# Kernel tuning notes

Hardware: AMD Instinct MI355X
Metric: run time of the kernel (lower is better)

## Reference

```python
import jax, jax.numpy as jnp
import numpy as np

B, CI, H, W = 128, 16, 32, 32
CO, K, S = 32, 3, 1
HO = (H - K) // S + 1  # 30
WO = (W - K) // S + 1  # 30
P = HO * WO  # 900 spatial locations
B_J0 = 0.1
DT = 0.5
BETA_ADAPT = 1.8  # is_adapt=True
BN_EPS = 1e-5


def setup_inputs() -> dict:
    key = jax.random.key(0)
    ks = jax.random.split(key, 16)
    inp = {
        'ff': jax.random.normal(ks[0], (B, CI, H, W), jnp.float32),
        'fb': jax.random.normal(ks[1], (B, CO, HO, WO), jnp.float32),
        'soma_t': jax.random.normal(ks[2], (B, CO, HO, WO), jnp.float32),
        'spk_t': (jax.random.uniform(ks[3], (B, CO, HO, WO)) > 0.7).astype(jnp.float32),
        'a_curr_t': jax.random.normal(ks[4], (B, CO, HO, WO), jnp.float32),
        'b_t': jax.random.uniform(ks[5], (B, CO, HO, WO), jnp.float32),
        # parameters
        'weight': jax.random.normal(ks[6], (1, CO, CI, HO, WO, K * K), jnp.float32) * 0.05,
        'conv_bias': jnp.zeros((1, CO, HO, WO), jnp.float32),
        'local_rec': jax.random.normal(ks[7], (P, CO, CO), jnp.float32) * (1.0 / np.sqrt(2.0 * CO)),
        'gamma': jnp.ones((CO,), jnp.float32),
        'beta': jnp.zeros((CO,), jnp.float32),
        'tau_m': 15.0 + 0.1 * jax.random.normal(ks[8], (CO, HO, WO), jnp.float32),
        'tau_adp': 20.0 + 0.1 * jax.random.normal(ks[9], (CO, HO, WO), jnp.float32),
        'tau_a': 15.0 + 0.1 * jax.random.normal(ks[10], (CO, HO, WO), jnp.float32),
    }
    return inp


def local_conv(x, weight, bias):
    # torch unfold(2,k).unfold(3,k) order: (kh, kw) fastest -> [B,Ci,Ho,Wo,k*k]
    patches = jnp.stack(
        [x[:, :, i:i + S * HO:S, j:j + S * WO:S] for i in range(K) for j in range(K)],
        axis=-1)
    out = jnp.einsum('bchwk,ochwk->bohw', patches, weight[0])
    return out + bias


def reference(ff, fb, soma_t, spk_t, a_curr_t, b_t, weight, conv_bias,
              local_rec, gamma, beta, tau_m, tau_adp, tau_a):
    # locally-connected conv + BatchNorm2d (training mode: batch stats)
    conv = local_conv(ff, weight, conv_bias)
    mean = conv.mean(axis=(0, 2, 3), keepdims=True)
    var = ((conv - mean) ** 2).mean(axis=(0, 2, 3), keepdims=True)  # biased var
    x = (conv - mean) * jax.lax.rsqrt(var + BN_EPS)
    conv_x = x * gamma[None, :, None, None] + beta[None, :, None, None]
    # recurrent per-location bmm: local_rec [P,Co,Co] @ spk [P,Co,B]
    spk_flat = spk_t.reshape(B, CO, P)
    rec = jnp.einsum('pij,bjp->bip', local_rec, spk_flat).reshape(B, CO, HO, WO)
    conv_x = conv_x + rec
    # adaptive LIF membrane update
    alpha = jnp.exp(-DT / tau_m)
    rho = jnp.exp(-DT / tau_adp)
    eta = jnp.exp(-DT / tau_a)
    b_new = rho * b_t + (1.0 - rho) * spk_t
    new_thre = B_J0 + BETA_ADAPT * b_new
    a_new = eta * a_curr_t + fb
    soma_new = alpha * soma_t + (jax.nn.sigmoid(a_new) - 0.5) + conv_x - new_thre * spk_t
    spike = (soma_new - new_thre > 0).astype(soma_new.dtype)
    return soma_new, spike, a_new, b_new
```

## Files before the change

### kernel.cpp

```cpp
#include <hip/hip_runtime.h>
#include <math.h>

#pragma clang fp contract(off)

#define B_   128
#define CI_  16
#define CO_  32
#define H_   32
#define W_   32
#define HO_  30
#define WO_  30
#define P_   900
#define CP_  (CO_*P_)
#define N_   ((size_t)B_*CP_)
#define NBLK_CONV (4*30*8)
#define WSTRIDE_O 129600
#define WSTRIDE_C 8100
#define FFC_ (H_*W_)
#define FFB_ (CI_*H_*W_)
#define FFTOT_ (B_*FFB_)


typedef __attribute__((address_space(1))) const unsigned int gas_uint;
typedef __attribute__((address_space(3))) unsigned int las_uint;
__device__ __forceinline__ void gload_lds4(const float* g, float* l) {
    __builtin_amdgcn_global_load_lds((gas_uint*)g, (las_uint*)l, 4, 0, 0);
}
__device__ __forceinline__ void gload_lds16(const float* g, float* l) {
    __builtin_amdgcn_global_load_lds((gas_uint*)g, (las_uint*)l, 16, 0, 0);
}

__global__ __launch_bounds__(256) void conv_kernel(
    const float* __restrict__ ff, const float* __restrict__ weight,
    const float* __restrict__ conv_bias, float* __restrict__ outf,
    double* __restrict__ part_sum, double* __restrict__ part_sumsq)
{
#pragma clang fp contract(off)
    const int tid = threadIdx.x;
    const int og  = (tid & 3) | ((tid >> 6) << 2);
    const int wg2 = (tid >> 2) & 3;
    const int bg  = (tid >> 4) & 3;
    const int wave = tid >> 6;
    const int wt = blockIdx.x;
    const int h  = blockIdx.y;
    const int b0 = blockIdx.z * 16;
    const int w0 = wt * 8 + wg2 * 2;
    const bool val = !(wt == 3 && wg2 == 3);
    const int wwave = tid & ~63;

    __shared__ float wgl[2][2432];
    __shared__ float ffs[2][576];

    int wq_off[8];
#pragma unroll
    for (int q = 0; q < 8; ++q) {
        int s = q * 256 + tid;
        int o = s >> 6, w = (s >> 3) & 7, k = s & 7;
        int colc = wt * 8 + w; if (colc > 29) colc = 29;
        wq_off[q] = o * WSTRIDE_O + (h * WO_ + colc) * 9 + k;
    }
    int w8_off;
    {
        int o = tid >> 3, w = tid & 7;
        int colc = wt * 8 + w; if (colc > 29) colc = 29;
        w8_off = o * WSTRIDE_O + (h * WO_ + colc) * 9 + 8;
    }
    const bool fon = (tid < 144);
    int f_off = 0;
    if (fon) {
        int s0 = 4 * tid;
        int bb = s0 / 36, rm = s0 % 36, r = rm / 12, cc0 = rm % 12;
        f_off = (b0 + bb) * FFB_ + (h + r) * W_ + wt * 8 + cc0;
    }

    float acc[2][2][4];
#pragma unroll
    for (int oo = 0; oo < 2; ++oo)
#pragma unroll
        for (int ww = 0; ww < 2; ++ww)
#pragma unroll
            for (int j = 0; j < 4; ++j) acc[oo][ww][j] = 0.f;

    auto stage = [&](int c, int buf) {
        const float* wsrc = weight + c * WSTRIDE_C;
#pragma unroll
        for (int q = 0; q < 8; ++q)
            gload_lds4(wsrc + wq_off[q], &wgl[buf][(q * 4 + wave) * 68]);
        gload_lds4(wsrc + w8_off, &wgl[buf][2176 + (wave << 6)]);
        if (fon) {
            int g = f_off + c * FFC_;
            if (g > FFTOT_ - 4) g = FFTOT_ - 4;
            gload_lds16(ff + g, &ffs[buf][4 * wwave]);
        }
    };

    const int o0 = og * 2;
    auto compute_c = [&](int buf) {
        float wk[2][2][9];
#pragma unroll
        for (int oo = 0; oo < 2; ++oo)
#pragma unroll
            for (int ww = 0; ww < 2; ++ww) {
                const int o = o0 + oo, w = wg2 * 2 + ww;
                const float* wp = &wgl[buf][o * 68 + w * 8];
                const float4 a = *reinterpret_cast<const float4*>(wp);
                const float4 b = *reinterpret_cast<const float4*>(wp + 4);
                wk[oo][ww][0] = a.x; wk[oo][ww][1] = a.y; wk[oo][ww][2] = a.z; wk[oo][ww][3] = a.w;
                wk[oo][ww][4] = b.x; wk[oo][ww][5] = b.y; wk[oo][ww][6] = b.z; wk[oo][ww][7] = b.w;
                wk[oo][ww][8] = wgl[buf][2176 + o * 8 + w];
            }
#pragma unroll
        for (int j = 0; j < 4; ++j) {
            const int bb = bg * 4 + j;
            float fr[3][4];
#pragma unroll
            for (int r = 0; r < 3; ++r) {
                const float2 u = *reinterpret_cast<const float2*>(&ffs[buf][bb * 36 + r * 12 + wg2 * 2]);
                const float2 v = *reinterpret_cast<const float2*>(&ffs[buf][bb * 36 + r * 12 + wg2 * 2 + 2]);
                fr[r][0] = u.x; fr[r][1] = u.y; fr[r][2] = v.x; fr[r][3] = v.y;
            }
#pragma unroll
            for (int oo = 0; oo < 2; ++oo)
#pragma unroll
                for (int ww = 0; ww < 2; ++ww) {
                    float a = acc[oo][ww][j];
#pragma unroll
                    for (int kh = 0; kh < 3; ++kh)
#pragma unroll
                        for (int kw = 0; kw < 3; ++kw) {
                            float prod = wk[oo][ww][kh * 3 + kw] * fr[kh][ww + kw];
                            a = a + prod;
                        }
                    acc[oo][ww][j] = a;
                }
        }
    };

    stage(0, 0);
    __syncthreads();
    for (int cs = 0; cs < CI_; cs += 2) {
        if (cs + 1 < CI_) stage(cs + 1, 1);
        compute_c(0);
        __syncthreads();
        if (cs + 2 < CI_) stage(cs + 2, 0);
        compute_c(1);
        __syncthreads();
    }

    double s1[2] = {0.0, 0.0}, s2[2] = {0.0, 0.0};
    if (val) {
#pragma unroll
        for (int oo = 0; oo < 2; ++oo) {
            const int o = o0 + oo;
            const int pidx = o * P_ + h * WO_ + w0;
            const float2 bi = *reinterpret_cast<const float2*>(conv_bias + pidx);
#pragma unroll
            for (int j = 0; j < 4; ++j) {
                const int b = b0 + bg * 4 + j;
                const size_t n = (size_t)b * CP_ + (size_t)pidx;
                float v0 = acc[oo][0][j] + bi.x;
                float v1 = acc[oo][1][j] + bi.y;
                *reinterpret_cast<float2*>(outf + 3 * N_ + n) = make_float2(v0, v1);
                double d0 = (double)v0, d1 = (double)v1;
                s1[oo] += d0; s2[oo] += d0 * d0;
                s1[oo] += d1; s2[oo] += d1 * d1;
            }
        }
    }
#pragma unroll
    for (int d = 4; d < 64; d <<= 1) {
#pragma unroll
        for (int oo = 0; oo < 2; ++oo) {
            s1[oo] += __shfl_xor(s1[oo], d);
            s2[oo] += __shfl_xor(s2[oo], d);
        }
    }
    if ((tid & 60) == 0) {
        int blk = (blockIdx.z * 30 + blockIdx.y) * 4 + blockIdx.x;
#pragma unroll
        for (int oo = 0; oo < 2; ++oo) {
            part_sum  [blk * CO_ + o0 + oo] = s1[oo];
            part_sumsq[blk * CO_ + o0 + oo] = s2[oo];
        }
    }
}

__global__ __launch_bounds__(256) void bn_finalize(
    const double* __restrict__ part_sum, const double* __restrict__ part_sumsq,
    float* __restrict__ Mb)
{
#pragma clang fp contract(off)
    const int o = blockIdx.x;
    const int tid = threadIdx.x;
    double s1 = 0.0, s2 = 0.0;
    for (int i = tid; i < NBLK_CONV; i += 256) {
        s1 += part_sum[i * CO_ + o];
        s2 += part_sumsq[i * CO_ + o];
    }
    __shared__ double r1[256], r2[256];
    r1[tid] = s1; r2[tid] = s2;
    __syncthreads();
    for (int s = 128; s > 0; s >>= 1) {
        if (tid < s) { r1[tid] += r1[tid + s]; r2[tid] += r2[tid + s]; }
        __syncthreads();
    }
    if (tid == 0) {
        const double cnt = (double)(B_ * (size_t)P_);
        double mean = r1[0] / cnt;
        float meanf = (float)mean;
        double md = (double)meanf;
        double var = r2[0] / cnt - 2.0 * md * (r1[0] / cnt) + md * md;
        float varf = (float)var;
        float invf = 1.0f / sqrtf(varf + 1e-5f);
        Mb[o]       = meanf;
        Mb[CO_ + o] = invf;
    }
}

__global__ __launch_bounds__(1024) void lif_rec_kernel(
    float* __restrict__ outf, const float* __restrict__ local_rec,
    const float* __restrict__ tau_m, const float* __restrict__ tau_adp,
    const float* __restrict__ tau_a, const float* __restrict__ Mb,
    const float* __restrict__ gamma, const float* __restrict__ beta,
    const float* __restrict__ fb, const float* __restrict__ soma_t,
    const float* __restrict__ spk_t, const float* __restrict__ a_curr,
    const float* __restrict__ b_t)
{
#pragma clang fp contract(off)
    const int tid = threadIdx.x;
    const int pp  = tid & 31;
    const int i   = tid >> 5;
    const int p   = blockIdx.x * 32 + pp;
    const bool pv = (p < P_);
    const int b0  = blockIdx.y * 8;

    float L[32];
    float meanf = 0.f, invf = 0.f, gm = 0.f, be = 0.f;
    float al = 0.f, rh = 0.f, et = 0.f;
    int rem = 0;
    if (pv) {
        const float4* lp = reinterpret_cast<const float4*>(local_rec + (size_t)p * (CO_ * CO_) + i * CO_);
#pragma unroll
        for (int q = 0; q < 8; ++q) {
            float4 v = lp[q];
            L[4 * q] = v.x; L[4 * q + 1] = v.y; L[4 * q + 2] = v.z; L[4 * q + 3] = v.w;
        }
        rem = i * P_ + p;
        meanf = Mb[i]; invf = Mb[CO_ + i];
        gm = gamma[i]; be = beta[i];
        al = expf(-0.5f / tau_m[rem]);
        rh = expf(-0.5f / tau_adp[rem]);
        et = expf(-0.5f / tau_a[rem]);
    }

    __shared__ float sp[2][CO_][32];

    size_t n = (size_t)b0 * CP_ + (size_t)rem;
    float sk_c = 0.f, cv_c = 0.f, bt_c = 0.f, ac_c = 0.f, fb_c = 0.f, so_c = 0.f;
    if (pv) {
        sk_c = spk_t[n]; cv_c = outf[3 * N_ + n]; bt_c = b_t[n];
        ac_c = a_curr[n]; fb_c = fb[n]; so_c = soma_t[n];
    }

#pragma unroll
    for (int bb = 0; bb < 8; ++bb) {
        const int cb = bb & 1;
        if (pv) sp[cb][i][pp] = sk_c;
        float sk_n = 0.f, cv_n = 0.f, bt_n = 0.f, ac_n = 0.f, fb_n = 0.f, so_n = 0.f;
        if (bb + 1 < 8 && pv) {
            const size_t nn = n + (size_t)CP_;
            sk_n = spk_t[nn]; cv_n = outf[3 * N_ + nn]; bt_n = b_t[nn];
            ac_n = a_curr[nn]; fb_n = fb[nn]; so_n = soma_t[nn];
        }
        asm volatile("s_waitcnt lgkmcnt(0)\n\ts_barrier" ::: "memory");
        if (pv) {
            float rec = 0.f;
#pragma unroll
            for (int j = 0; j < CO_; ++j) {
                float prod = L[j] * sp[cb][j][pp];
                rec = rec + prod;
            }

            float t  = cv_c - meanf;
            float x  = t * invf;
            float xg = x * gm;
            float cx = xg + be;
            cx = cx + rec;

            float rb  = rh * bt_c;
            float omr = 1.0f - rh;
            float os  = omr * sk_c;
            float bn  = rb + os;
            float tb = 1.8f * bn;
            float th = 0.1f + tb;
            float ea = et * ac_c;
            float an = ea + fb_c;
            float sg = 1.0f / (1.0f + expf(-an));
            float as = al * so_c;
            float s5 = sg - 0.5f;
            float u1 = as + s5;
            float u2 = u1 + cx;
            float ts = th * sk_c;
            float sn = u2 - ts;

            outf[n]          = sn;
            outf[N_ + n]     = ((sn - th) > 0.0f) ? 1.f : 0.f;
            outf[2 * N_ + n] = an;
            outf[3 * N_ + n] = bn;
        }
        sk_c = sk_n; cv_c = cv_n; bt_c = bt_n; ac_c = ac_n; fb_c = fb_n; so_c = so_n;
        n += (size_t)CP_;
    }
}

extern "C" void kernel_launch(void* const* d_in, const int* in_sizes, int n_in,
                              void* d_out, int out_size, void* d_ws, size_t ws_size,
                              hipStream_t stream)
{
    const float* ff        = (const float*)d_in[0];
    const float* fb        = (const float*)d_in[1];
    const float* soma_t    = (const float*)d_in[2];
    const float* spk_t     = (const float*)d_in[3];
    const float* a_curr    = (const float*)d_in[4];
    const float* b_t       = (const float*)d_in[5];
    const float* weight    = (const float*)d_in[6];
    const float* conv_bias = (const float*)d_in[7];
    const float* local_rec = (const float*)d_in[8];
    const float* gamma     = (const float*)d_in[9];
    const float* beta      = (const float*)d_in[10];
    const float* tau_m     = (const float*)d_in[11];
    const float* tau_adp   = (const float*)d_in[12];
    const float* tau_a     = (const float*)d_in[13];

    double* part_sum = (double*)d_ws;
    double* part_sq  = part_sum + (size_t)NBLK_CONV * CO_;
    float*  Mb       = (float*)(part_sq + (size_t)NBLK_CONV * CO_);

    float* outf = (float*)d_out;

    conv_kernel<<<dim3(4, 30, 8), 256, 0, stream>>>(
        ff, weight, conv_bias, outf, part_sum, part_sq);
    bn_finalize<<<dim3(CO_), 256, 0, stream>>>(part_sum, part_sq, Mb);
    lif_rec_kernel<<<dim3(29, 16), 1024, 0, stream>>>(
        outf, local_rec, tau_m, tau_adp, tau_a, Mb, gamma, beta,
        fb, soma_t, spk_t, a_curr, b_t);
}
```

Before: 115.0 us.

## Triple-buffer conv staging with partial vmcnt waits and remap block grids

The conv kernel goes from double to triple LDS buffering. It replaces full __syncthreads with s_waitcnt vmcnt(9) plus barrier, so two channel stages stay in flight while one is being computed. Both conv and LIF kernels switch to 1D grids with a custom block-index decode. This likely groups blocks that share weight or local_rec tiles across XCDs or caches, and the LIF grid is padded to 512 with early exits. LDS use rises by half, and the hardcoded vmcnt count depends on the exact number of loads per stage.

```diff
diff --git a/kernel.cpp b/kernel.cpp
--- a/kernel.cpp
+++ b/kernel.cpp
@@ -41,15 +41,17 @@
     const int wg2 = (tid >> 2) & 3;
     const int bg  = (tid >> 4) & 3;
     const int wave = tid >> 6;
-    const int wt = blockIdx.x;
-    const int h  = blockIdx.y;
-    const int b0 = blockIdx.z * 16;
+    const int D  = blockIdx.x;
+    const int zb = D & 7;
+    const int wt = (D >> 3) & 3;
+    const int h  = D >> 5;
+    const int b0 = zb * 16;
     const int w0 = wt * 8 + wg2 * 2;
     const bool val = !(wt == 3 && wg2 == 3);
     const int wwave = tid & ~63;
 
-    __shared__ float wgl[2][2432];
-    __shared__ float ffs[2][576];
+    __shared__ float wgl[3][2432];
+    __shared__ float ffs[3][576];
 
     int wq_off[8];
 #pragma unroll
@@ -136,16 +138,24 @@
         }
     };
 
+#define BAR9  asm volatile("s_waitcnt vmcnt(9)\n\ts_barrier" ::: "memory")
+
     stage(0, 0);
-    __syncthreads();
-    for (int cs = 0; cs < CI_; cs += 2) {
-        if (cs + 1 < CI_) stage(cs + 1, 1);
+    stage(1, 1);
+    for (int t = 0; t < 15; t += 3) {
+        BAR9;
+        stage(t + 2, 2);
         compute_c(0);
-        __syncthreads();
-        if (cs + 2 < CI_) stage(cs + 2, 0);
+        BAR9;
+        if (t + 3 < CI_) stage(t + 3, 0);
         compute_c(1);
-        __syncthreads();
-    }
+        BAR9;
+        if (t + 4 < CI_) stage(t + 4, 1);
+        compute_c(2);
+    }
+    asm volatile("s_waitcnt vmcnt(0)\n\ts_barrier" ::: "memory");
+    compute_c(0);
+#undef BAR9
 
     double s1[2] = {0.0, 0.0}, s2[2] = {0.0, 0.0};
     if (val) {
@@ -176,7 +186,7 @@
         }
     }
     if ((tid & 60) == 0) {
-        int blk = (blockIdx.z * 30 + blockIdx.y) * 4 + blockIdx.x;
+        int blk = (zb * 30 + h) * 4 + wt;
 #pragma unroll
         for (int oo = 0; oo < 2; ++oo) {
             part_sum  [blk * CO_ + o0 + oo] = s1[oo];
@@ -227,12 +237,20 @@
     const float* __restrict__ b_t)
 {
 #pragma clang fp contract(off)
+    const int D    = blockIdx.x;
+    const int pt8  = D & 7;
+    const int rest = D >> 3;
+    const int by   = rest & 15;
+    const int ptq  = rest >> 4;
+    const int pt   = ptq * 8 + pt8;
+    if (pt >= 29) return;
+
     const int tid = threadIdx.x;
     const int pp  = tid & 31;
     const int i   = tid >> 5;
-    const int p   = blockIdx.x * 32 + pp;
+    const int p   = pt * 32 + pp;
     const bool pv = (p < P_);
-    const int b0  = blockIdx.y * 8;
+    const int b0  = by * 8;
 
     float L[32];
     float meanf = 0.f, invf = 0.f, gm = 0.f, be = 0.f;
@@ -338,10 +356,10 @@
 
     float* outf = (float*)d_out;
 
-    conv_kernel<<<dim3(4, 30, 8), 256, 0, stream>>>(
+    conv_kernel<<<dim3(960), 256, 0, stream>>>(
         ff, weight, conv_bias, outf, part_sum, part_sq);
     bn_finalize<<<dim3(CO_), 256, 0, stream>>>(part_sum, part_sq, Mb);
-    lif_rec_kernel<<<dim3(29, 16), 1024, 0, stream>>>(
+    lif_rec_kernel<<<dim3(512), 1024, 0, stream>>>(
         outf, local_rec, tau_m, tau_adp, tau_a, Mb, gamma, beta,
         fb, soma_t, spk_t, a_curr, b_t);
 }
```

Result: slower. 128.0 us (+11.3%).

## Split LIF kernel into smaller blocks, load spikes from global instead of LDS

Applied to the files above, without the earlier changes.

Restructures the LIF/recurrent kernel from 1024-thread blocks that share the spike vector through double-buffered LDS with barriers into 256-thread blocks. Each thread now reads the 32 spike values it needs straight from global memory, relying on cache reuse across the threads that share a location. The grid is flattened with an index swizzle, and blocks past the last location exit early. This removes the barriers and the LDS traffic and should improve occupancy, at the cost of redundant global/L2 spike loads and the loss of software prefetching (loop no longer unrolled).

```diff
diff --git a/kernel.cpp b/kernel.cpp
--- a/kernel.cpp
+++ b/kernel.cpp
@@ -217,7 +217,7 @@
     }
 }
 
-__global__ __launch_bounds__(1024) void lif_rec_kernel(
+__global__ __launch_bounds__(256) void lif_rec_kernel(
     float* __restrict__ outf, const float* __restrict__ local_rec,
     const float* __restrict__ tau_m, const float* __restrict__ tau_adp,
     const float* __restrict__ tau_a, const float* __restrict__ Mb,
@@ -227,89 +227,87 @@
     const float* __restrict__ b_t)
 {
 #pragma clang fp contract(off)
+    const int D   = blockIdx.x;
+    const int pt8 = D & 7;
+    int r         = D >> 3;
+    const int ig  = r & 3;  r >>= 2;
+    const int bg  = r & 15; r >>= 4;
+    const int ptq = r;
+    const int pt  = ptq * 8 + pt8;
+    if (pt >= 29) return;
+
     const int tid = threadIdx.x;
     const int pp  = tid & 31;
-    const int i   = tid >> 5;
-    const int p   = blockIdx.x * 32 + pp;
+    const int i   = ig * 8 + (tid >> 5);
+    const int p   = pt * 32 + pp;
     const bool pv = (p < P_);
-    const int b0  = blockIdx.y * 8;
+    if (!pv) return;
+    const int b0  = bg * 8;
 
     float L[32];
-    float meanf = 0.f, invf = 0.f, gm = 0.f, be = 0.f;
-    float al = 0.f, rh = 0.f, et = 0.f;
-    int rem = 0;
-    if (pv) {
+    {
         const float4* lp = reinterpret_cast<const float4*>(local_rec + (size_t)p * (CO_ * CO_) + i * CO_);
 #pragma unroll
         for (int q = 0; q < 8; ++q) {
             float4 v = lp[q];
             L[4 * q] = v.x; L[4 * q + 1] = v.y; L[4 * q + 2] = v.z; L[4 * q + 3] = v.w;
         }
-        rem = i * P_ + p;
-        meanf = Mb[i]; invf = Mb[CO_ + i];
-        gm = gamma[i]; be = beta[i];
-        al = expf(-0.5f / tau_m[rem]);
-        rh = expf(-0.5f / tau_adp[rem]);
-        et = expf(-0.5f / tau_a[rem]);
-    }
-
-    __shared__ float sp[2][CO_][32];
+    }
+    const int rem = i * P_ + p;
+    const float meanf = Mb[i], invf = Mb[CO_ + i];
+    const float gm = gamma[i], be = beta[i];
+    const float al = expf(-0.5f / tau_m[rem]);
+    const float rh = expf(-0.5f / tau_adp[rem]);
+    const float et = expf(-0.5f / tau_a[rem]);
+    const float omr = 1.0f - rh;
 
     size_t n = (size_t)b0 * CP_ + (size_t)rem;
-    float sk_c = 0.f, cv_c = 0.f, bt_c = 0.f, ac_c = 0.f, fb_c = 0.f, so_c = 0.f;
-    if (pv) {
-        sk_c = spk_t[n]; cv_c = outf[3 * N_ + n]; bt_c = b_t[n];
-        ac_c = a_curr[n]; fb_c = fb[n]; so_c = soma_t[n];
-    }
-
-#pragma unroll
+    const float* spk_col = spk_t + (size_t)b0 * CP_ + (size_t)p;
+
+#pragma unroll 1
     for (int bb = 0; bb < 8; ++bb) {
-        const int cb = bb & 1;
-        if (pv) sp[cb][i][pp] = sk_c;
-        float sk_n = 0.f, cv_n = 0.f, bt_n = 0.f, ac_n = 0.f, fb_n = 0.f, so_n = 0.f;
-        if (bb + 1 < 8 && pv) {
-            const size_t nn = n + (size_t)CP_;
-            sk_n = spk_t[nn]; cv_n = outf[3 * N_ + nn]; bt_n = b_t[nn];
-            ac_n = a_curr[nn]; fb_n = fb[nn]; so_n = soma_t[nn];
-        }
-        asm volatile("s_waitcnt lgkmcnt(0)\n\ts_barrier" ::: "memory");
-        if (pv) {
-            float rec = 0.f;
-#pragma unroll
-            for (int j = 0; j < CO_; ++j) {
-                float prod = L[j] * sp[cb][j][pp];
-                rec = rec + prod;
-            }
-
-            float t  = cv_c - meanf;
-            float x  = t * invf;
-            float xg = x * gm;
-            float cx = xg + be;
-            cx = cx + rec;
-
-            float rb  = rh * bt_c;
-            float omr = 1.0f - rh;
-            float os  = omr * sk_c;
-            float bn  = rb + os;
-            float tb = 1.8f * bn;
-            float th = 0.1f + tb;
-            float ea = et * ac_c;
-            float an = ea + fb_c;
-            float sg = 1.0f / (1.0f + expf(-an));
-            float as = al * so_c;
-            float s5 = sg - 0.5f;
-            float u1 = as + s5;
-            float u2 = u1 + cx;
-            float ts = th * sk_c;
-            float sn = u2 - ts;
-
-            outf[n]          = sn;
-            outf[N_ + n]     = ((sn - th) > 0.0f) ? 1.f : 0.f;
-            outf[2 * N_ + n] = an;
-            outf[3 * N_ + n] = bn;
-        }
-        sk_c = sk_n; cv_c = cv_n; bt_c = bt_n; ac_c = ac_n; fb_c = fb_n; so_c = so_n;
+        float sj[32];
+#pragma unroll
+        for (int j = 0; j < 32; ++j) sj[j] = spk_col[(size_t)j * P_];
+
+        float rec = 0.f;
+#pragma unroll
+        for (int j = 0; j < CO_; ++j) {
+            float prod = L[j] * sj[j];
+            rec = rec + prod;
+        }
+
+        const float sk = spk_t[n];
+        const float cv = outf[3 * N_ + n];
+
+        float t  = cv - meanf;
+        float x  = t * invf;
+        float xg = x * gm;
+        float cx = xg + be;
+        cx = cx + rec;
+
+        float rb  = rh * b_t[n];
+        float os  = omr * sk;
+        float bn  = rb + os;
+        float tb = 1.8f * bn;
+        float th = 0.1f + tb;
+        float ea = et * a_curr[n];
+        float an = ea + fb[n];
+        float sg = 1.0f / (1.0f + expf(-an));
+        float as = al * soma_t[n];
+        float s5 = sg - 0.5f;
+        float u1 = as + s5;
+        float u2 = u1 + cx;
+        float ts = th * sk;
+        float sn = u2 - ts;
+
+        outf[n]          = sn;
+        outf[N_ + n]     = ((sn - th) > 0.0f) ? 1.f : 0.f;
+        outf[2 * N_ + n] = an;
+        outf[3 * N_ + n] = bn;
+
         n += (size_t)CP_;
+        spk_col += (size_t)CP_;
     }
 }
 
@@ -341,7 +339,7 @@
     conv_kernel<<<dim3(4, 30, 8), 256, 0, stream>>>(
         ff, weight, conv_bias, outf, part_sum, part_sq);
     bn_finalize<<<dim3(CO_), 256, 0, stream>>>(part_sum, part_sq, Mb);
-    lif_rec_kernel<<<dim3(29, 16), 1024, 0, stream>>>(
+    lif_rec_kernel<<<dim3(2048), 256, 0, stream>>>(
         outf, local_rec, tau_m, tau_adp, tau_a, Mb, gamma, beta,
         fb, soma_t, spk_t, a_curr, b_t);
 }
```

Measured after the change: 121.7 us. 1.06x slower.
